# Performance work log

Measured on AMD Instinct MI355X. Metric: run time of the kernel, lower is better.

## Reference

```python
import jax, jax.numpy as jnp
import numpy as np

D_MODEL = 512
N_HEAD = 8
D_HEAD = D_MODEL // N_HEAD
EPS = 1e-6


def setup_inputs() -> dict:
    key = jax.random.key(0)
    ks = jax.random.split(key, 11)
    b, s, d = 4, 8192, D_MODEL
    scale = 1.0 / np.sqrt(d)
    inp = {
        "q": jax.random.normal(ks[0], (b, s, d), jnp.float32),
        "k": jax.random.normal(ks[1], (b, s, d), jnp.float32),
        "v": jax.random.normal(ks[2], (b, s, d), jnp.float32),
        "Wq": jax.random.normal(ks[3], (d, d), jnp.float32) * scale,
        "bq": jax.random.normal(ks[4], (d,), jnp.float32) * 0.01,
        "Wk": jax.random.normal(ks[5], (d, d), jnp.float32) * scale,
        "bk": jax.random.normal(ks[6], (d,), jnp.float32) * 0.01,
        "Wv": jax.random.normal(ks[7], (d, d), jnp.float32) * scale,
        "bv": jax.random.normal(ks[8], (d,), jnp.float32) * 0.01,
        "Wo": jax.random.normal(ks[9], (d, d), jnp.float32) * scale,
        "bo": jax.random.normal(ks[10], (d,), jnp.float32) * 0.01,
    }
    return inp


def reference(q, k, v, Wq, bq, Wk, bk, Wv, bv, Wo, bo):
    b, s, d = q.shape
    # torch nn.Linear: x @ W.T + b
    feat = lambda x, W, bias: jax.nn.elu(
        (x @ W.T + bias).reshape(b, s, N_HEAD, D_HEAD)) + 1.0
    queries = feat(q, Wq, bq)                      # [b,s,h,dh]
    keys = feat(k, Wk, bk)                         # [b,s,h,dh]
    values = (v @ Wv.T + bv).reshape(b, s, N_HEAD, D_HEAD)
    # full-sequence KV summary state
    k_v = jnp.einsum('bshd,bshm->bhdm', keys, values)   # [b,h,dh,dh]
    z = keys.sum(axis=1, keepdims=True)                 # [b,1,h,dh]
    num = jnp.einsum('bshd,bhdm->bshm', queries, k_v)   # [b,s,h,dh]
    den = jnp.sum(queries * z, axis=-1)                 # [b,s,h] (broadcast over s)
    out = num / (den[..., None] + EPS)
    out = out.reshape(b, s, d)
    return (out @ Wo.T + bo, k_v, z)
```

## Files before the change

### kernel.cpp

```cpp
#include <hip/hip_runtime.h>
#include <hip/hip_bf16.h>
#include <stdint.h>

typedef __bf16 bf16x8 __attribute__((ext_vector_type(8)));
typedef float f32x4 __attribute__((ext_vector_type(4)));

#define S_LEN 8192
#define BATCH 4
#define DMODEL 512
#define NHEAD 8
#define DHEAD 64
#define MROWS (BATCH * S_LEN)
#define OUT0_ELEMS (MROWS * DMODEL)
#define KV_ELEMS (BATCH * NHEAD * DHEAD * DHEAD)
#define Z_ELEMS (BATCH * NHEAD * DHEAD)

#define WAITV6() asm volatile("s_waitcnt vmcnt(6)" ::: "memory")
#define WAITV4() asm volatile("s_waitcnt vmcnt(4)" ::: "memory")
#define WAITV2() asm volatile("s_waitcnt vmcnt(2)" ::: "memory")
#define WAITV0() asm volatile("s_waitcnt vmcnt(0)" ::: "memory")
#define WAITL0() asm volatile("s_waitcnt lgkmcnt(0)" ::: "memory")
#define BARRIER() do { asm volatile("" ::: "memory"); \
                       __builtin_amdgcn_s_barrier(); \
                       asm volatile("" ::: "memory"); } while (0)

__device__ __forceinline__ uint16_t f2bf(float f) {
    uint32_t u = __float_as_uint(f);
    u = (u + 0x7fffu + ((u >> 16) & 1u)) >> 16;
    return (uint16_t)u;
}
__device__ __forceinline__ uint32_t pack2(float a, float b) {
    union { __hip_bfloat162 h; uint32_t u; } cv;
    cv.h = __float22bfloat162_rn(make_float2(a, b));
    return cv.u;
}
__device__ __forceinline__ void gload_lds16(const void* g, void* l) {
    __builtin_amdgcn_global_load_lds(
        (const __attribute__((address_space(1))) void*)g,
        (__attribute__((address_space(3))) void*)l, 16, 0, 0);
}

__global__ void wconv_kernel(const float* __restrict__ w0, const float* __restrict__ w1,
                             const float* __restrict__ w2, const float* __restrict__ w3,
                             uint16_t* __restrict__ dst) {
    const float* src = (blockIdx.y == 0) ? w0 : (blockIdx.y == 1) ? w1
                       : (blockIdx.y == 2) ? w2 : w3;
    uint16_t* d = dst + (size_t)blockIdx.y * (DMODEL * DMODEL);
    int i = (blockIdx.x * 256 + threadIdx.x) * 4;
    float4 v = *(const float4*)(src + i);
    uint2 o;
    o.x = pack2(v.x, v.y);
    o.y = pack2(v.z, v.w);
    *(uint2*)(d + i) = o;
}

__global__ __launch_bounds__(256, 3)
void gemm_qkv_kernel(const float* __restrict__ qp, const float* __restrict__ kp,
                     const float* __restrict__ vp, const uint16_t* __restrict__ Wb,
                     const float* __restrict__ bq, const float* __restrict__ bk,
                     const float* __restrict__ bv,
                     uint16_t* __restrict__ Qb, uint16_t* __restrict__ KT,
                     uint16_t* __restrict__ VT)
{
    __shared__ uint4 smem4[2048];
    uint16_t* sAb[2] = {(uint16_t*)smem4, (uint16_t*)smem4 + 8192};
    uint16_t* sBb[2] = {(uint16_t*)smem4 + 4096, (uint16_t*)smem4 + 12288};
    const int tid = threadIdx.x;
    const int lane = tid & 63, w = tid >> 6;
    const int quad = lane >> 4, l15 = lane & 15;
    const int which = blockIdx.y >> 2;
    const int m_blk = blockIdx.x * 128, n_blk = (blockIdx.y & 3) * 128;
    const int g0 = w * 2;

    const float* Af = (which == 0) ? qp : (which == 1) ? kp : vp;
    const float* bias = (which == 0) ? bq : (which == 1) ? bk : bv;
    const uint16_t* Wm = Wb + (size_t)which * 262144;

    f32x4 acc[4][4];
#pragma unroll
    for (int mi = 0; mi < 4; ++mi)
#pragma unroll
        for (int ni = 0; ni < 4; ++ni) acc[mi][ni] = (f32x4){0.f, 0.f, 0.f, 0.f};

    const int ar = tid >> 1;
    const int ah = tid & 1;
    const float* arow_base = Af + (size_t)(m_blk + ar) * 512 + ah * 16;

    auto loadA = [&](int t, float4* r) {
        const float* p = arow_base + t * 32;
        r[0] = *(const float4*)(p);
        r[1] = *(const float4*)(p + 4);
        r[2] = *(const float4*)(p + 8);
        r[3] = *(const float4*)(p + 12);
    };
    auto packA = [&](uint16_t* sA, const float4* r) {
        uint16_t* base = sA + (((ar >> 4) * 4 + ah * 2) * 16 + (ar & 15)) * 8;
        *(uint4*)base = make_uint4(pack2(r[0].x, r[0].y), pack2(r[0].z, r[0].w),
                                   pack2(r[1].x, r[1].y), pack2(r[1].z, r[1].w));
        *(uint4*)(base + 128) = make_uint4(pack2(r[2].x, r[2].y), pack2(r[2].z, r[2].w),
                                           pack2(r[3].x, r[3].y), pack2(r[3].z, r[3].w));
    };
    auto stageB = [&](uint16_t* sB, int t) {
        const int k0 = t * 32;
        gload_lds16(Wm + (size_t)(n_blk + g0 * 16 + l15) * 512 + k0 + quad * 8,
                    sB + g0 * 512);
        gload_lds16(Wm + (size_t)(n_blk + (g0 + 1) * 16 + l15) * 512 + k0 + quad * 8,
                    sB + (g0 + 1) * 512);
    };
    auto compute = [&](const uint16_t* sA, const uint16_t* sB) {
        bf16x8 afr[4], bfr[4];
#pragma unroll
        for (int mi = 0; mi < 4; ++mi)
            afr[mi] = *(const bf16x8*)(sA + (((w & 1) * 4 + mi) * 64 + lane) * 8);
#pragma unroll
        for (int ni = 0; ni < 4; ++ni)
            bfr[ni] = *(const bf16x8*)(sB + (((w >> 1) * 4 + ni) * 64 + lane) * 8);
#pragma unroll
        for (int mi = 0; mi < 4; ++mi)
#pragma unroll
            for (int ni = 0; ni < 4; ++ni)
                acc[mi][ni] = __builtin_amdgcn_mfma_f32_16x16x32_bf16(
                    afr[mi], bfr[ni], acc[mi][ni], 0, 0, 0);
    };

    float4 rA[2][4];
    stageB(sBb[0], 0);
    loadA(0, rA[0]);
    packA(sAb[0], rA[0]);
    loadA(1, rA[1]);

#pragma unroll
    for (int t = 0; t < 16; ++t) {
        const int cur = t & 1, nxt = cur ^ 1;
        if (t < 15) stageB(sBb[nxt], t + 1);
        if (t < 14) loadA(t + 2, rA[cur]);
        if (t < 15) packA(sAb[nxt], rA[nxt]);
        if (t < 14)      { WAITV6(); }
        else if (t == 14){ WAITV2(); }
        else             { WAITV0(); }
        WAITL0();
        BARRIER();
        compute(sAb[cur], sBb[cur]);
        BARRIER();
    }
    __syncthreads();

    const int mw = (w & 1) * 64, nw = (w >> 1) * 64;
    const bool elu = (which != 2);
    float bias4[4];
#pragma unroll
    for (int ni = 0; ni < 4; ++ni) bias4[ni] = bias[n_blk + nw + ni * 16 + l15];

    if (which == 0) {
        uint16_t* t = (uint16_t*)smem4 + w * 2048;
        uint16_t* C = Qb;
#pragma unroll
        for (int mi = 0; mi < 4; ++mi) {
#pragma unroll
            for (int ni = 0; ni < 4; ++ni)
#pragma unroll
                for (int r = 0; r < 4; ++r) {
                    float val = acc[mi][ni][r] + bias4[ni];
                    val = (val > 0.f) ? (val + 1.f) : __expf(val);
                    t[(quad * 4 + r) * 64 + ni * 16 + l15] = f2bf(val);
                }
#pragma unroll
            for (int c = 0; c < 2; ++c) {
                const int idx = c * 64 + lane;
                const int row = idx >> 3, colc = (idx & 7) * 8;
                uint4 vv = *(const uint4*)(t + row * 64 + colc);
                *(uint4*)(C + (size_t)(m_blk + mw + mi * 16 + row) * 512
                            + n_blk + nw + colc) = vv;
            }
        }
    } else {
        uint16_t* t = (uint16_t*)smem4 + w * 2560;
        uint16_t* C = (which == 1) ? KT : VT;
        const int bb = m_blk >> 13;
        const int s_base = (m_blk & 8191) + mw;
#pragma unroll
        for (int p = 0; p < 2; ++p) {
#pragma unroll
            for (int mi2 = 0; mi2 < 2; ++mi2) {
                const int mi = p * 2 + mi2;
#pragma unroll
                for (int ni = 0; ni < 4; ++ni)
#pragma unroll
                    for (int r = 0; r < 4; ++r) {
                        float val = acc[mi][ni][r] + bias4[ni];
                        if (elu) val = (val > 0.f) ? (val + 1.f) : __expf(val);
                        t[(ni * 16 + l15) * 40 + mi2 * 16 + quad * 4 + r] = f2bf(val);
                    }
            }
#pragma unroll
            for (int it = 0; it < 4; ++it) {
                const int idx = it * 64 + lane;
                const int col = idx >> 2, sg = idx & 3;
                uint4 vv = *(const uint4*)(t + col * 40 + sg * 8);
                *(uint4*)(C + ((size_t)(bb * 512) + n_blk + nw + col) * 8192
                            + s_base + p * 32 + sg * 8) = vv;
            }
        }
    }
}

__global__ __launch_bounds__(256, 3)
void gemm_out_kernel(const uint16_t* __restrict__ Ab, const uint16_t* __restrict__ Wm,
                     const float* __restrict__ bias, float* __restrict__ C)
{
    __shared__ uint4 smem4[2048];
    uint16_t* sAb[2] = {(uint16_t*)smem4, (uint16_t*)smem4 + 8192};
    uint16_t* sBb[2] = {(uint16_t*)smem4 + 4096, (uint16_t*)smem4 + 12288};
    const int tid = threadIdx.x;
    const int lane = tid & 63, w = tid >> 6;
    const int quad = lane >> 4, l15 = lane & 15;
    const int m_blk = blockIdx.x * 128, n_blk = blockIdx.y * 128;
    const int g0 = w * 2;

    f32x4 acc[4][4];
#pragma unroll
    for (int mi = 0; mi < 4; ++mi)
#pragma unroll
        for (int ni = 0; ni < 4; ++ni) acc[mi][ni] = (f32x4){0.f, 0.f, 0.f, 0.f};

    auto stageA = [&](uint16_t* sA, int t) {
        const int k0 = t * 32;
        gload_lds16(Ab + (size_t)(m_blk + g0 * 16 + l15) * 512 + k0 + quad * 8,
                    sA + g0 * 512);
        gload_lds16(Ab + (size_t)(m_blk + (g0 + 1) * 16 + l15) * 512 + k0 + quad * 8,
                    sA + (g0 + 1) * 512);
    };
    auto stageB = [&](uint16_t* sB, int t) {
        const int k0 = t * 32;
        gload_lds16(Wm + (size_t)(n_blk + g0 * 16 + l15) * 512 + k0 + quad * 8,
                    sB + g0 * 512);
        gload_lds16(Wm + (size_t)(n_blk + (g0 + 1) * 16 + l15) * 512 + k0 + quad * 8,
                    sB + (g0 + 1) * 512);
    };
    auto compute = [&](const uint16_t* sA, const uint16_t* sB) {
        bf16x8 afr[4], bfr[4];
#pragma unroll
        for (int mi = 0; mi < 4; ++mi)
            afr[mi] = *(const bf16x8*)(sA + (((w & 1) * 4 + mi) * 64 + lane) * 8);
#pragma unroll
        for (int ni = 0; ni < 4; ++ni)
            bfr[ni] = *(const bf16x8*)(sB + (((w >> 1) * 4 + ni) * 64 + lane) * 8);
#pragma unroll
        for (int mi = 0; mi < 4; ++mi)
#pragma unroll
            for (int ni = 0; ni < 4; ++ni)
                acc[mi][ni] = __builtin_amdgcn_mfma_f32_16x16x32_bf16(
                    afr[mi], bfr[ni], acc[mi][ni], 0, 0, 0);
    };

    stageA(sAb[0], 0);
    stageB(sBb[0], 0);
#pragma unroll
    for (int t = 0; t < 16; ++t) {
        const int cur = t & 1, nxt = cur ^ 1;
        if (t < 15) { stageA(sAb[nxt], t + 1); stageB(sBb[nxt], t + 1); }
        if (t < 15) { WAITV4(); } else { WAITV0(); }
        BARRIER();
        compute(sAb[cur], sBb[cur]);
        BARRIER();
    }
    __syncthreads();

    const int mw = (w & 1) * 64, nw = (w >> 1) * 64;
    float bias4[4];
#pragma unroll
    for (int ni = 0; ni < 4; ++ni) bias4[ni] = bias[n_blk + nw + ni * 16 + l15];

    float* t = (float*)(smem4 + w * 256);
#pragma unroll
    for (int mi = 0; mi < 4; ++mi) {
#pragma unroll
        for (int ni = 0; ni < 4; ++ni)
#pragma unroll
            for (int r = 0; r < 4; ++r)
                t[(quad * 4 + r) * 64 + ni * 16 + l15] = acc[mi][ni][r] + bias4[ni];
#pragma unroll
        for (int c = 0; c < 4; ++c) {
            const int idx = c * 64 + lane;
            const int row = idx >> 4, colc = (idx & 15) * 4;
            float4 vv = *(const float4*)(t + row * 64 + colc);
            *(float4*)(C + (size_t)(m_blk + mw + mi * 16 + row) * 512
                         + n_blk + nw + colc) = vv;
        }
    }
}

__global__ __launch_bounds__(256, 4)
void kv_kernel(const uint16_t* __restrict__ KT, const uint16_t* __restrict__ VT,
               float* __restrict__ kvz)
{
    const int tid = threadIdx.x;
    const int lane = tid & 63, w = tid >> 6;
    const int quad = lane >> 4, l15 = lane & 15;
    const int bh = blockIdx.y, b = bh >> 3, h = bh & 7;
    const int dh2 = w & 1, mh2 = w >> 1;
    const int S0 = blockIdx.x * 512;

    const uint16_t* Ka[2];
    const uint16_t* Va[2];
#pragma unroll
    for (int i = 0; i < 2; ++i) {
        Ka[i] = KT + (size_t)(b * 512 + h * 64 + dh2 * 32 + i * 16 + l15) * 8192 + S0 + quad * 8;
        Va[i] = VT + (size_t)(b * 512 + h * 64 + mh2 * 32 + i * 16 + l15) * 8192 + S0 + quad * 8;
    }

    f32x4 acc[2][2], accz[2];
#pragma unroll
    for (int mi = 0; mi < 2; ++mi) {
        accz[mi] = (f32x4){0.f, 0.f, 0.f, 0.f};
#pragma unroll
        for (int ni = 0; ni < 2; ++ni) acc[mi][ni] = (f32x4){0.f, 0.f, 0.f, 0.f};
    }
    bf16x8 ones;
#pragma unroll
    for (int j = 0; j < 8; ++j) ones[j] = (__bf16)1.0f;

    uint4 ka[2], va[2];
#pragma unroll
    for (int i = 0; i < 2; ++i) {
        ka[i] = *(const uint4*)(Ka[i]);
        va[i] = *(const uint4*)(Va[i]);
    }

#pragma unroll
    for (int it = 0; it < 16; ++it) {
        uint4 kn[2], vn[2];
        if (it < 15) {
#pragma unroll
            for (int i = 0; i < 2; ++i) {
                kn[i] = *(const uint4*)(Ka[i] + (it + 1) * 32);
                vn[i] = *(const uint4*)(Va[i] + (it + 1) * 32);
            }
        }
        bf16x8 afr[2], bfr[2];
#pragma unroll
        for (int i = 0; i < 2; ++i) {
            union { uint4 u; bf16x8 v; } ca, cb;
            ca.u = ka[i]; afr[i] = ca.v;
            cb.u = va[i]; bfr[i] = cb.v;
        }
#pragma unroll
        for (int mi = 0; mi < 2; ++mi)
#pragma unroll
            for (int ni = 0; ni < 2; ++ni)
                acc[mi][ni] = __builtin_amdgcn_mfma_f32_16x16x32_bf16(
                    afr[mi], bfr[ni], acc[mi][ni], 0, 0, 0);
        if (mh2 == 0) {
#pragma unroll
            for (int mi = 0; mi < 2; ++mi)
                accz[mi] = __builtin_amdgcn_mfma_f32_16x16x32_bf16(
                    afr[mi], ones, accz[mi], 0, 0, 0);
        }
        if (it < 15) {
#pragma unroll
            for (int i = 0; i < 2; ++i) { ka[i] = kn[i]; va[i] = vn[i]; }
        }
    }
    float* kvp = kvz + (size_t)bh * 4096;
#pragma unroll
    for (int mi = 0; mi < 2; ++mi)
#pragma unroll
        for (int ni = 0; ni < 2; ++ni)
#pragma unroll
            for (int r = 0; r < 4; ++r)
                atomicAdd(kvp + (dh2 * 32 + mi * 16 + quad * 4 + r) * 64
                              + mh2 * 32 + ni * 16 + l15, acc[mi][ni][r]);
    if (mh2 == 0 && l15 == 0) {
#pragma unroll
        for (int mi = 0; mi < 2; ++mi)
#pragma unroll
            for (int r = 0; r < 4; ++r)
                atomicAdd(kvz + KV_ELEMS + bh * 64 + dh2 * 32 + mi * 16 + quad * 4 + r,
                          accz[mi][r]);
    }
}

__global__ void kvf_kernel(const float* __restrict__ kvz, uint16_t* __restrict__ KVf) {
    const int bh = blockIdx.x;
    const int tid = threadIdx.x;
    for (int e = tid; e < 5120; e += 256) {
        const int j = e & 7, c = e >> 3;
        const int l15c = c & 15, quadc = (c >> 4) & 3, kkc = (c >> 6) & 1, ng = c >> 7;
        const int n = ng * 16 + l15c;
        const int d = kkc * 32 + quadc * 8 + j;
        float val = (n < 64) ? kvz[(size_t)bh * 4096 + d * 64 + n]
                  : ((n == 64) ? kvz[KV_ELEMS + bh * 64 + d] : 0.f);
        KVf[(size_t)bh * 5120 + e] = f2bf(val);
    }
}

__global__ __launch_bounds__(256, 4)
void attn_kernel(const uint16_t* __restrict__ Qb, const uint16_t* __restrict__ KVf,
                 uint16_t* __restrict__ Yb)
{
    __shared__ uint4 smem4[1152];
    uint16_t* sB = (uint16_t*)smem4;
    uint16_t* sEp = (uint16_t*)(smem4 + 640);
    const int bh = blockIdx.y;
    const int b = bh >> 3, h = bh & 7;
    const int tid = threadIdx.x;
    const int lane = tid & 63, w = tid >> 6, quad = lane >> 4, l15 = lane & 15;

    const uint16_t* src = KVf + (size_t)bh * 5120;
    gload_lds16(src + (size_t)tid * 8,         sB + (w * 64) * 8);
    gload_lds16(src + (size_t)(256 + tid) * 8, sB + ((256 + w * 64)) * 8);
    if (tid < 128)
        gload_lds16(src + (size_t)(512 + tid) * 8, sB + ((512 + w * 64)) * 8);
    __syncthreads();

    f32x4 acc[2][5];
#pragma unroll
    for (int mi = 0; mi < 2; ++mi)
#pragma unroll
        for (int ni = 0; ni < 5; ++ni) acc[mi][ni] = (f32x4){0.f, 0.f, 0.f, 0.f};
    const int row0 = blockIdx.x * 128 + w * 32;
#pragma unroll
    for (int kk = 0; kk < 2; ++kk) {
        bf16x8 afr[2];
#pragma unroll
        for (int mi = 0; mi < 2; ++mi) {
            const size_t ga = (size_t)(b * S_LEN + row0 + mi * 16 + l15) * DMODEL
                              + h * DHEAD + kk * 32 + quad * 8;
            afr[mi] = *(const bf16x8*)(Qb + ga);
        }
#pragma unroll
        for (int ni = 0; ni < 5; ++ni) {
            bf16x8 bfr = *(const bf16x8*)(sB + ((ni * 2 + kk) * 64 + lane) * 8);
            acc[0][ni] = __builtin_amdgcn_mfma_f32_16x16x32_bf16(afr[0], bfr, acc[0][ni], 0, 0, 0);
            acc[1][ni] = __builtin_amdgcn_mfma_f32_16x16x32_bf16(afr[1], bfr, acc[1][ni], 0, 0, 0);
        }
    }
    uint16_t* t = sEp + w * 1024;
#pragma unroll
    for (int mi = 0; mi < 2; ++mi) {
        float rden[4];
#pragma unroll
        for (int r = 0; r < 4; ++r) {
            const float den = __shfl(acc[mi][4][r], lane & 48, 64);
            rden[r] = 1.0f / (den + 1e-6f);
        }
#pragma unroll
        for (int ni = 0; ni < 4; ++ni)
#pragma unroll
            for (int r = 0; r < 4; ++r)
                t[(quad * 4 + r) * 64 + ni * 16 + l15] = f2bf(acc[mi][ni][r] * rden[r]);
#pragma unroll
        for (int c = 0; c < 2; ++c) {
            const int idx = c * 64 + lane;
            const int row = idx >> 3, colc = (idx & 7) * 8;
            uint4 vv = *(const uint4*)(t + row * 64 + colc);
            *(uint4*)(Yb + (size_t)(b * S_LEN + row0 + mi * 16 + row) * 512
                        + h * DHEAD + colc) = vv;
        }
    }
}

extern "C" void kernel_launch(void* const* d_in, const int* in_sizes, int n_in,
                              void* d_out, int out_size, void* d_ws, size_t ws_size,
                              hipStream_t stream)
{
    const float* q  = (const float*)d_in[0];
    const float* k  = (const float*)d_in[1];
    const float* v  = (const float*)d_in[2];
    const float* Wq = (const float*)d_in[3];
    const float* bq = (const float*)d_in[4];
    const float* Wk = (const float*)d_in[5];
    const float* bk = (const float*)d_in[6];
    const float* Wv = (const float*)d_in[7];
    const float* bv = (const float*)d_in[8];
    const float* Wo = (const float*)d_in[9];
    const float* bo = (const float*)d_in[10];

    uint16_t* Qb = (uint16_t*)d_ws;
    uint16_t* KT = Qb + OUT0_ELEMS;
    uint16_t* VT = KT + OUT0_ELEMS;
    uint16_t* Wb = VT + OUT0_ELEMS;
    uint16_t* KVf = VT;
    uint16_t* Yb = KT;

    float* out0 = (float*)d_out;
    float* kvz  = out0 + OUT0_ELEMS;

    hipMemsetAsync(kvz, 0, (KV_ELEMS + Z_ELEMS) * sizeof(float), stream);
    wconv_kernel<<<dim3(256, 4), 256, 0, stream>>>(Wq, Wk, Wv, Wo, Wb);
    gemm_qkv_kernel<<<dim3(256, 12), 256, 0, stream>>>(q, k, v, Wb, bq, bk, bv,
                                                       Qb, KT, VT);
    kv_kernel<<<dim3(16, 32), 256, 0, stream>>>(KT, VT, kvz);
    kvf_kernel<<<dim3(32), 256, 0, stream>>>(kvz, KVf);
    attn_kernel<<<dim3(64, 32), 256, 0, stream>>>(Qb, KVf, Yb);
    gemm_out_kernel<<<dim3(256, 4), 256, 0, stream>>>(Yb, Wb + 3 * 262144, bo, out0);
}
```

Baseline: 377.7 us.

## Triple-buffer LDS in QKV and output GEMMs to drop second barrier

Both GEMM kernels move from double-buffered to triple-buffered LDS stages. Loads are prefetched two k-steps ahead and issued after the barrier, which lets each iteration use one barrier instead of two. The goal is to hide more global-load latency and cut synchronisation stalls. In exchange, LDS per block grows from 32KB to 48KB, which may limit occupancy against the launch bound of 3 blocks, and the QKV kernel holds an extra register buffer for A.

New measurement: 396.9 us. +5.1%, slower.

```diff
diff --git a/kernel.cpp b/kernel.cpp
--- a/kernel.cpp
+++ b/kernel.cpp
@@ -15,10 +15,7 @@
 #define KV_ELEMS (BATCH * NHEAD * DHEAD * DHEAD)
 #define Z_ELEMS (BATCH * NHEAD * DHEAD)
 
-#define WAITV6() asm volatile("s_waitcnt vmcnt(6)" ::: "memory")
-#define WAITV4() asm volatile("s_waitcnt vmcnt(4)" ::: "memory")
-#define WAITV2() asm volatile("s_waitcnt vmcnt(2)" ::: "memory")
-#define WAITV0() asm volatile("s_waitcnt vmcnt(0)" ::: "memory")
+#define WAITV(n) asm volatile("s_waitcnt vmcnt(" #n ")" ::: "memory")
 #define WAITL0() asm volatile("s_waitcnt lgkmcnt(0)" ::: "memory")
 #define BARRIER() do { asm volatile("" ::: "memory"); \
                        __builtin_amdgcn_s_barrier(); \
@@ -62,9 +59,8 @@
                      uint16_t* __restrict__ Qb, uint16_t* __restrict__ KT,
                      uint16_t* __restrict__ VT)
 {
-    __shared__ uint4 smem4[2048];
-    uint16_t* sAb[2] = {(uint16_t*)smem4, (uint16_t*)smem4 + 8192};
-    uint16_t* sBb[2] = {(uint16_t*)smem4 + 4096, (uint16_t*)smem4 + 12288};
+    __shared__ uint4 smem4[3072];
+    uint16_t* const sbase = (uint16_t*)smem4;
     const int tid = threadIdx.x;
     const int lane = tid & 63, w = tid >> 6;
     const int quad = lane >> 4, l15 = lane & 15;
@@ -86,6 +82,9 @@
     const int ah = tid & 1;
     const float* arow_base = Af + (size_t)(m_blk + ar) * 512 + ah * 16;
 
+    auto sAs = [&](int s) { return sbase + s * 8192; };
+    auto sBs = [&](int s) { return sbase + s * 8192 + 4096; };
+
     auto loadA = [&](int t, float4* r) {
         const float* p = arow_base + t * 32;
         r[0] = *(const float4*)(p);
@@ -123,25 +122,26 @@
                     afr[mi], bfr[ni], acc[mi][ni], 0, 0, 0);
     };
 
-    float4 rA[2][4];
-    stageB(sBb[0], 0);
+    float4 rA[3][4];
+    stageB(sBs(0), 0);
     loadA(0, rA[0]);
-    packA(sAb[0], rA[0]);
+    stageB(sBs(1), 1);
     loadA(1, rA[1]);
+    loadA(2, rA[2]);
+    packA(sAs(0), rA[0]);
 
 #pragma unroll
     for (int t = 0; t < 16; ++t) {
-        const int cur = t & 1, nxt = cur ^ 1;
-        if (t < 15) stageB(sBb[nxt], t + 1);
-        if (t < 14) loadA(t + 2, rA[cur]);
-        if (t < 15) packA(sAb[nxt], rA[nxt]);
-        if (t < 14)      { WAITV6(); }
-        else if (t == 14){ WAITV2(); }
-        else             { WAITV0(); }
+        if (t == 0 || t == 1) { WAITV(14); }
+        else if (t <= 13)     { WAITV(10); }
+        else if (t == 14)     { WAITV(6); }
+        else                  { WAITV(0); }
         WAITL0();
         BARRIER();
-        compute(sAb[cur], sBb[cur]);
-        BARRIER();
+        if (t <= 13) stageB(sBs((t + 2) % 3), t + 2);
+        if (t <= 12) loadA(t + 3, rA[t % 3]);
+        if (t <= 14) packA(sAs((t + 1) % 3), rA[(t + 1) % 3]);
+        compute(sAs(t % 3), sBs(t % 3));
     }
     __syncthreads();
 
@@ -208,9 +208,8 @@
 void gemm_out_kernel(const uint16_t* __restrict__ Ab, const uint16_t* __restrict__ Wm,
                      const float* __restrict__ bias, float* __restrict__ C)
 {
-    __shared__ uint4 smem4[2048];
-    uint16_t* sAb[2] = {(uint16_t*)smem4, (uint16_t*)smem4 + 8192};
-    uint16_t* sBb[2] = {(uint16_t*)smem4 + 4096, (uint16_t*)smem4 + 12288};
+    __shared__ uint4 smem4[3072];
+    uint16_t* const sbase = (uint16_t*)smem4;
     const int tid = threadIdx.x;
     const int lane = tid & 63, w = tid >> 6;
     const int quad = lane >> 4, l15 = lane & 15;
@@ -222,6 +221,9 @@
     for (int mi = 0; mi < 4; ++mi)
 #pragma unroll
         for (int ni = 0; ni < 4; ++ni) acc[mi][ni] = (f32x4){0.f, 0.f, 0.f, 0.f};
+
+    auto sAs = [&](int s) { return sbase + s * 8192; };
+    auto sBs = [&](int s) { return sbase + s * 8192 + 4096; };
 
     auto stageA = [&](uint16_t* sA, int t) {
         const int k0 = t * 32;
@@ -253,16 +255,16 @@
                     afr[mi], bfr[ni], acc[mi][ni], 0, 0, 0);
     };
 
-    stageA(sAb[0], 0);
-    stageB(sBb[0], 0);
+    stageA(sAs(0), 0); stageB(sBs(0), 0);
+    stageA(sAs(1), 1); stageB(sBs(1), 1);
+
 #pragma unroll
     for (int t = 0; t < 16; ++t) {
-        const int cur = t & 1, nxt = cur ^ 1;
-        if (t < 15) { stageA(sAb[nxt], t + 1); stageB(sBb[nxt], t + 1); }
-        if (t < 15) { WAITV4(); } else { WAITV0(); }
+        if (t <= 14) { WAITV(4); } else { WAITV(0); }
+        WAITL0();
         BARRIER();
-        compute(sAb[cur], sBb[cur]);
-        BARRIER();
+        if (t <= 13) { stageA(sAs((t + 2) % 3), t + 2); stageB(sBs((t + 2) % 3), t + 2); }
+        compute(sAs(t % 3), sBs(t % 3));
     }
     __syncthreads();
 
```
